# Kernel tuning notes

Hardware: AMD Instinct MI355X
Metric: run time of the kernel (lower is better)

The kernel has to match this reference:

```python
import jax, jax.numpy as jnp
import numpy as np

B, S, D = 4, 2048, 512
H, DK, DV = 8, 64, 64
LN_EPS = 1e-5


def setup_inputs() -> dict:
    key = jax.random.key(0)
    ks = jax.random.split(key, 9)
    inp = {
        "input_Q": jax.random.normal(ks[0], (B, S, D), jnp.float32),
        "input_K": jax.random.normal(ks[1], (B, S, D), jnp.float32),
        "input_V": jax.random.normal(ks[2], (B, S, D), jnp.float32),
        "attn_mask": jax.random.bernoulli(ks[3], 0.1, (B, S, S)),
        # weights stored [in, out] (math-equivalent to torch Linear's x @ W.T)
        "W_Q": jax.random.normal(ks[4], (D, H * DK), jnp.float32) * (1.0 / np.sqrt(D)),
        "W_K": jax.random.normal(ks[5], (D, H * DK), jnp.float32) * (1.0 / np.sqrt(D)),
        "W_V": jax.random.normal(ks[6], (D, H * DV), jnp.float32) * (1.0 / np.sqrt(D)),
        "W_fc": jax.random.normal(ks[7], (H * DV, D), jnp.float32) * (1.0 / np.sqrt(H * DV)),
        "ln_gamma": jnp.ones((D,), jnp.float32),
        "ln_beta": jnp.zeros((D,), jnp.float32),
    }
    return inp


def _mha(input_Q, input_K, input_V, attn_mask, W_Q, W_K, W_V, W_fc, ln_gamma, ln_beta):
    # project and split heads -> [B, H, S, d]
    Q = (input_Q @ W_Q).reshape(B, S, H, DK).transpose(0, 2, 1, 3)
    K = (input_K @ W_K).reshape(B, S, H, DK).transpose(0, 2, 1, 3)
    V = (input_V @ W_V).reshape(B, S, H, DV).transpose(0, 2, 1, 3)
    # scaled dot-product attention with masking (mask broadcast over heads)
    scores = jnp.einsum('bhqd,bhkd->bhqk', Q, K) / np.sqrt(DK)
    scores = jnp.where(attn_mask[:, None, :, :], -1e9, scores)
    attn = jax.nn.softmax(scores, axis=-1)
    context = jnp.einsum('bhqk,bhkd->bhqd', attn, V)
    context = context.transpose(0, 2, 1, 3).reshape(B, S, H * DV)
    out = context @ W_fc + input_Q  # fc + residual
    # LayerNorm over last dim
    mu = jnp.mean(out, axis=-1, keepdims=True)
    var = jnp.var(out, axis=-1, keepdims=True)
    normed = (out - mu) * jax.lax.rsqrt(var + LN_EPS) * ln_gamma + ln_beta
    return normed, attn


def reference(input_Q, input_K, input_V, attn_mask, W_Q, W_K, W_V, W_fc, ln_gamma, ln_beta):
    return _mha(input_Q, input_K, input_V, attn_mask, W_Q, W_K, W_V, W_fc, ln_gamma, ln_beta)
```

## Files before the change

kernel.cpp:

```cpp
#include <hip/hip_runtime.h>
#include <stdint.h>

typedef __attribute__((ext_vector_type(8))) short short8;
typedef __attribute__((ext_vector_type(4))) float f32x4;
typedef __attribute__((ext_vector_type(16))) float f32x16;
typedef __attribute__((ext_vector_type(4))) unsigned short ushort4v;
typedef __attribute__((ext_vector_type(4))) int int4v;

__device__ __forceinline__ unsigned short f2bf(float f) {
    union { float f; uint32_t u; } v; v.f = f;
    return (unsigned short)((v.u + 0x7FFFu + ((v.u >> 16) & 1u)) >> 16);
}
__device__ __forceinline__ float bf2f(unsigned short h) {
    union { uint32_t u; float f; } v; v.u = ((uint32_t)h) << 16;
    return v.f;
}

__global__ __launch_bounds__(256) void prep_wt_kernel(
    const float* __restrict__ W0, const float* __restrict__ W1,
    const float* __restrict__ W2, const float* __restrict__ W3,
    unsigned short* __restrict__ Wt)
{
    __shared__ unsigned short tile[64][66];
    const float* W = blockIdx.y == 0 ? W0 : blockIdx.y == 1 ? W1 : blockIdx.y == 2 ? W2 : W3;
    unsigned short* dst = Wt + (size_t)blockIdx.y * (512 * 512);
    const int k0 = (blockIdx.x >> 3) * 64;
    const int n0 = (blockIdx.x & 7) * 64;
    const int nx = threadIdx.x & 63;
    const int ty = threadIdx.x >> 6;
#pragma unroll
    for (int i = 0; i < 16; ++i) {
        const int kl = i * 4 + ty;
        tile[nx][kl] = f2bf(W[(size_t)(k0 + kl) * 512 + n0 + nx]);
    }
    __syncthreads();
#pragma unroll
    for (int i = 0; i < 16; ++i) {
        const int nl = i * 4 + ty;
        dst[(size_t)(n0 + nl) * 512 + k0 + nx] = tile[nl][nx];
    }
}

__global__ __launch_bounds__(256) void proj_kernel(
    const float* __restrict__ inQ, const float* __restrict__ inK, const float* __restrict__ inV,
    const unsigned short* __restrict__ Wt,
    unsigned short* __restrict__ outQ, unsigned short* __restrict__ outK,
    unsigned short* __restrict__ outVT)
{
    const int which = blockIdx.y;
    const float* inp = which == 0 ? inQ : which == 1 ? inK : inV;
    const unsigned short* Wtb = Wt + (size_t)which * (512 * 512);
    const int tid = threadIdx.x;
    const int wid = tid >> 6, l = tid & 63;
    const int rt = wid >> 1, ch = wid & 1;
    const int lrow = l & 15, g = l >> 4;
    const int rowbase = blockIdx.x * 32;
    const int arow = rowbase + rt * 16 + lrow;

    f32x4 acc[16];
#pragma unroll
    for (int t = 0; t < 16; ++t) acc[t] = (f32x4){0.f, 0.f, 0.f, 0.f};

    for (int k0 = 0; k0 < 512; k0 += 32) {
        const float* ap = inp + (size_t)arow * 512 + k0 + g * 8;
        float4 a0 = *(const float4*)ap;
        float4 a1 = *(const float4*)(ap + 4);
        short8 af;
        af[0] = (short)f2bf(a0.x); af[1] = (short)f2bf(a0.y);
        af[2] = (short)f2bf(a0.z); af[3] = (short)f2bf(a0.w);
        af[4] = (short)f2bf(a1.x); af[5] = (short)f2bf(a1.y);
        af[6] = (short)f2bf(a1.z); af[7] = (short)f2bf(a1.w);
#pragma unroll
        for (int t = 0; t < 16; ++t) {
            const int n = ch * 256 + t * 16 + lrow;
            short8 bf = *(const short8*)(Wtb + (size_t)n * 512 + k0 + g * 8);
            acc[t] = __builtin_amdgcn_mfma_f32_16x16x32_bf16(af, bf, acc[t], 0, 0, 0);
        }
    }

    if (which == 2) {
#pragma unroll
        for (int t = 0; t < 16; ++t) {
            const int n = ch * 256 + t * 16 + lrow;
            const int hh = n >> 6, dd = n & 63;
            const int row0 = rowbase + rt * 16 + g * 4;
            const int bb = row0 >> 11, s0 = row0 & 2047;
            ushort4v pk;
            pk[0] = f2bf(acc[t][0]); pk[1] = f2bf(acc[t][1]);
            pk[2] = f2bf(acc[t][2]); pk[3] = f2bf(acc[t][3]);
            *(ushort4v*)(outVT + ((size_t)(bb * 8 + hh) * 64 + dd) * 2048 + s0) = pk;
        }
    } else {
        unsigned short* dst = which == 0 ? outQ : outK;
#pragma unroll
        for (int t = 0; t < 16; ++t) {
            const int n = ch * 256 + t * 16 + lrow;
            const int hh = n >> 6, dd = n & 63;
#pragma unroll
            for (int r = 0; r < 4; ++r) {
                const int row = rowbase + rt * 16 + g * 4 + r;
                const int bb = row >> 11, s0 = row & 2047;
                dst[((size_t)(bb * 8 + hh) * 2048 + s0) * 64 + dd] = f2bf(acc[t][r]);
            }
        }
    }
}

__global__ __launch_bounds__(256, 4) void attn_kernel(
    const unsigned short* __restrict__ Qw, const unsigned short* __restrict__ Kw,
    const unsigned short* __restrict__ VT, const unsigned char* __restrict__ mask,
    float* __restrict__ attn_out, float* __restrict__ ctx)
{
    __shared__ float psum_lds[4][32];
    __shared__ float ctx_lds[4][32][67];

    const int L = blockIdx.x;
    const int xcd = L & 7, j = L >> 3;
    const int bh = xcd * 4 + (j >> 6);
    const int qb = j & 63;
    const int b = bh >> 3, h = bh & 7;
    const int qg0 = qb * 32;
    const int tid = threadIdx.x, wid = tid >> 6, l = tid & 63;
    const int lq = l & 31, hi = l >> 5;
    const float EXPC = 0.18033688011112042f;

    const unsigned short* qbase = Qw + ((size_t)bh * 2048 + qg0 + lq) * 64 + 8 * hi;
    short8 qf[4];
#pragma unroll
    for (int d4 = 0; d4 < 4; ++d4) qf[d4] = *(const short8*)(qbase + d4 * 16);

    const int k0w = wid * 512;
    const unsigned char* mbase = mask + ((size_t)b * 2048 + qg0 + lq) * 2048 + 4 * hi;
    const unsigned short* kwb = Kw + ((size_t)bh * 2048 + lq) * 64 + 8 * hi;

    float psum = 0.f;
    for (int t = 0; t < 16; ++t) {
        const int kb = k0w + t * 32;
        const unsigned short* kp = kwb + (size_t)kb * 64;
        short8 kf0 = *(const short8*)(kp);
        short8 kf1 = *(const short8*)(kp + 16);
        short8 kf2 = *(const short8*)(kp + 32);
        short8 kf3 = *(const short8*)(kp + 48);
        f32x16 sc = (f32x16)(0.f);
        sc = __builtin_amdgcn_mfma_f32_32x32x16_bf16(kf0, qf[0], sc, 0, 0, 0);
        sc = __builtin_amdgcn_mfma_f32_32x32x16_bf16(kf1, qf[1], sc, 0, 0, 0);
        sc = __builtin_amdgcn_mfma_f32_32x32x16_bf16(kf2, qf[2], sc, 0, 0, 0);
        sc = __builtin_amdgcn_mfma_f32_32x32x16_bf16(kf3, qf[3], sc, 0, 0, 0);
#pragma unroll
        for (int c2 = 0; c2 < 4; ++c2) {
            const uint32_t m4 = *(const uint32_t*)(mbase + kb + 8 * c2);
#pragma unroll
            for (int rr = 0; rr < 4; ++rr) {
                const float e = ((m4 >> (8 * rr)) & 255u) ? 0.f
                                : exp2f(sc[c2 * 4 + rr] * EXPC);
                psum += e;
            }
        }
    }
    psum += __shfl_xor(psum, 32);
    if (l < 32) psum_lds[wid][l] = psum;
    __syncthreads();
    const float rinv = 1.0f / (psum_lds[0][lq] + psum_lds[1][lq] +
                               psum_lds[2][lq] + psum_lds[3][lq]);

    f32x16 acc0 = (f32x16)(0.f), acc1 = (f32x16)(0.f);
    float* abase = attn_out + ((size_t)bh * 2048 + qg0 + lq) * 2048 + 4 * hi;
    const unsigned short* vb0 = VT + ((size_t)bh * 64 + lq) * 2048 + 8 * hi;
    const unsigned short* vb1 = vb0 + (size_t)32 * 2048;

    for (int t = 0; t < 16; ++t) {
        const int kb = k0w + t * 32;
        const unsigned short* kp = kwb + (size_t)kb * 64;
        short8 kf0 = *(const short8*)(kp);
        short8 kf1 = *(const short8*)(kp + 16);
        short8 kf2 = *(const short8*)(kp + 32);
        short8 kf3 = *(const short8*)(kp + 48);
        f32x16 sc = (f32x16)(0.f);
        sc = __builtin_amdgcn_mfma_f32_32x32x16_bf16(kf0, qf[0], sc, 0, 0, 0);
        sc = __builtin_amdgcn_mfma_f32_32x32x16_bf16(kf1, qf[1], sc, 0, 0, 0);
        sc = __builtin_amdgcn_mfma_f32_32x32x16_bf16(kf2, qf[2], sc, 0, 0, 0);
        sc = __builtin_amdgcn_mfma_f32_32x32x16_bf16(kf3, qf[3], sc, 0, 0, 0);

        float e[16];
#pragma unroll
        for (int c2 = 0; c2 < 4; ++c2) {
            const uint32_t m4 = *(const uint32_t*)(mbase + kb + 8 * c2);
#pragma unroll
            for (int rr = 0; rr < 4; ++rr) {
                e[c2 * 4 + rr] = ((m4 >> (8 * rr)) & 255u) ? 0.f
                                 : exp2f(sc[c2 * 4 + rr] * EXPC) * rinv;
            }
        }
#pragma unroll
        for (int c2 = 0; c2 < 4; ++c2) {
            float4 st = {e[c2 * 4 + 0], e[c2 * 4 + 1], e[c2 * 4 + 2], e[c2 * 4 + 3]};
            *(float4*)(abase + kb + 8 * c2) = st;
        }
#pragma unroll
        for (int kh = 0; kh < 2; ++kh) {
            const int cA = 2 * kh, cB = 2 * kh + 1;
            uint32_t w0 = (uint32_t)f2bf(e[4 * cA + 0]) | ((uint32_t)f2bf(e[4 * cA + 1]) << 16);
            uint32_t w1 = (uint32_t)f2bf(e[4 * cB + 0]) | ((uint32_t)f2bf(e[4 * cB + 1]) << 16);
            uint32_t w2 = (uint32_t)f2bf(e[4 * cA + 2]) | ((uint32_t)f2bf(e[4 * cA + 3]) << 16);
            uint32_t w3 = (uint32_t)f2bf(e[4 * cB + 2]) | ((uint32_t)f2bf(e[4 * cB + 3]) << 16);
            asm("v_permlane32_swap_b32 %0, %1" : "+v"(w0), "+v"(w1));
            asm("v_permlane32_swap_b32 %0, %1" : "+v"(w2), "+v"(w3));
            int4v pw = {(int)w0, (int)w2, (int)w1, (int)w3};
            short8 pb = *(short8*)&pw;
            const size_t voff = (size_t)(kb + 16 * kh);
            short8 v0 = *(const short8*)(vb0 + voff);
            short8 v1 = *(const short8*)(vb1 + voff);
            acc0 = __builtin_amdgcn_mfma_f32_32x32x16_bf16(v0, pb, acc0, 0, 0, 0);
            acc1 = __builtin_amdgcn_mfma_f32_32x32x16_bf16(v1, pb, acc1, 0, 0, 0);
        }
    }

#pragma unroll
    for (int r = 0; r < 16; ++r) {
        const int d = (r & 3) + 8 * (r >> 2) + 4 * hi;
        ctx_lds[wid][lq][d] = acc0[r];
        ctx_lds[wid][lq][d + 32] = acc1[r];
    }
    __syncthreads();
#pragma unroll
    for (int i = 0; i < 8; ++i) {
        const int idx = i * 256 + tid;
        const int q = idx >> 6, d = idx & 63;
        const float s = ctx_lds[0][q][d] + ctx_lds[1][q][d] +
                        ctx_lds[2][q][d] + ctx_lds[3][q][d];
        ctx[((size_t)b * 2048 + qg0 + q) * 512 + h * 64 + d] = s;
    }
}

__global__ __launch_bounds__(256) void fc_ln_kernel(
    const float* __restrict__ ctx, const unsigned short* __restrict__ Wtfc,
    const float* __restrict__ resid, const float* __restrict__ gamma,
    const float* __restrict__ beta, float* __restrict__ out)
{
    __shared__ float red[32][2][2];
    const int tid = threadIdx.x;
    const int wid = tid >> 6, l = tid & 63;
    const int rt = wid >> 1, ch = wid & 1;
    const int lrow = l & 15, g = l >> 4;
    const int rowbase = blockIdx.x * 32;
    const int arow = rowbase + rt * 16 + lrow;

    f32x4 acc[16];
#pragma unroll
    for (int t = 0; t < 16; ++t) acc[t] = (f32x4){0.f, 0.f, 0.f, 0.f};

    for (int k0 = 0; k0 < 512; k0 += 32) {
        const float* ap = ctx + (size_t)arow * 512 + k0 + g * 8;
        float4 a0 = *(const float4*)ap;
        float4 a1 = *(const float4*)(ap + 4);
        short8 af;
        af[0] = (short)f2bf(a0.x); af[1] = (short)f2bf(a0.y);
        af[2] = (short)f2bf(a0.z); af[3] = (short)f2bf(a0.w);
        af[4] = (short)f2bf(a1.x); af[5] = (short)f2bf(a1.y);
        af[6] = (short)f2bf(a1.z); af[7] = (short)f2bf(a1.w);
#pragma unroll
        for (int t = 0; t < 16; ++t) {
            const int n = ch * 256 + t * 16 + lrow;
            short8 bf = *(const short8*)(Wtfc + (size_t)n * 512 + k0 + g * 8);
            acc[t] = __builtin_amdgcn_mfma_f32_16x16x32_bf16(af, bf, acc[t], 0, 0, 0);
        }
    }

    float s1[4] = {0,0,0,0}, s2[4] = {0,0,0,0};
#pragma unroll
    for (int t = 0; t < 16; ++t) {
        const int n = ch * 256 + t * 16 + lrow;
#pragma unroll
        for (int r = 0; r < 4; ++r) {
            const int row = rowbase + rt * 16 + g * 4 + r;
            float v = acc[t][r] + resid[(size_t)row * 512 + n];
            acc[t][r] = v;
            s1[r] += v;
            s2[r] += v * v;
        }
    }
#pragma unroll
    for (int r = 0; r < 4; ++r) {
        s1[r] += __shfl_xor(s1[r], 1); s2[r] += __shfl_xor(s2[r], 1);
        s1[r] += __shfl_xor(s1[r], 2); s2[r] += __shfl_xor(s2[r], 2);
        s1[r] += __shfl_xor(s1[r], 4); s2[r] += __shfl_xor(s2[r], 4);
        s1[r] += __shfl_xor(s1[r], 8); s2[r] += __shfl_xor(s2[r], 8);
    }
    if (lrow == 0) {
#pragma unroll
        for (int r = 0; r < 4; ++r) {
            red[rt * 16 + g * 4 + r][ch][0] = s1[r];
            red[rt * 16 + g * 4 + r][ch][1] = s2[r];
        }
    }
    __syncthreads();
    float mean[4], rstd[4];
#pragma unroll
    for (int r = 0; r < 4; ++r) {
        const int rl = rt * 16 + g * 4 + r;
        const float S1 = red[rl][0][0] + red[rl][1][0];
        const float S2 = red[rl][0][1] + red[rl][1][1];
        mean[r] = S1 * (1.0f / 512.0f);
        const float var = S2 * (1.0f / 512.0f) - mean[r] * mean[r];
        rstd[r] = rsqrtf(var + 1e-5f);
    }
#pragma unroll
    for (int t = 0; t < 16; ++t) {
        const int n = ch * 256 + t * 16 + lrow;
        const float gm = gamma[n], bt = beta[n];
#pragma unroll
        for (int r = 0; r < 4; ++r) {
            const int row = rowbase + rt * 16 + g * 4 + r;
            out[(size_t)row * 512 + n] = (acc[t][r] - mean[r]) * rstd[r] * gm + bt;
        }
    }
}

extern "C" void kernel_launch(void* const* d_in, const int* in_sizes, int n_in,
                              void* d_out, int out_size, void* d_ws, size_t ws_size,
                              hipStream_t stream)
{
    (void)in_sizes; (void)n_in; (void)out_size; (void)ws_size;
    const float* inQ = (const float*)d_in[0];
    const float* inK = (const float*)d_in[1];
    const float* inV = (const float*)d_in[2];
    const unsigned char* mask = (const unsigned char*)d_in[3];
    const float* WQ  = (const float*)d_in[4];
    const float* WK  = (const float*)d_in[5];
    const float* WV  = (const float*)d_in[6];
    const float* Wfc = (const float*)d_in[7];
    const float* gamma = (const float*)d_in[8];
    const float* beta  = (const float*)d_in[9];

    char* ws = (char*)d_ws;
    unsigned short* wsQ   = (unsigned short*)(ws);
    unsigned short* wsK   = (unsigned short*)(ws + ((size_t)8  << 20));
    unsigned short* wsVT  = (unsigned short*)(ws + ((size_t)16 << 20));
    float*          wsCtx = (float*)         (ws + ((size_t)24 << 20));
    unsigned short* wsWt  = (unsigned short*)(ws + ((size_t)40 << 20));

    float* out_ln   = (float*)d_out;
    float* out_attn = out_ln + (size_t)4 * 2048 * 512;

    prep_wt_kernel<<<dim3(64, 4), dim3(256), 0, stream>>>(WQ, WK, WV, Wfc, wsWt);
    proj_kernel<<<dim3(256, 3), dim3(256), 0, stream>>>(inQ, inK, inV, wsWt, wsQ, wsK, wsVT);
    attn_kernel<<<dim3(2048), dim3(256), 0, stream>>>(wsQ, wsK, wsVT, mask,
                                                      out_attn, wsCtx);
    fc_ln_kernel<<<dim3(256), dim3(256), 0, stream>>>(wsCtx, wsWt + (size_t)3 * 512 * 512,
                                                      inQ, gamma, beta, out_ln);
}
```

Before: 1.002 ms.

## Split projection and fc grids, use raw exp/cvt asm, tree-reduce attention context

The projection kernel gains a second grid dimension that splits the output columns in half, and the fc+LayerNorm kernel processes 16 rows per block across four waves, doubling the block count of both GEMMs for better CU occupancy. In the attention kernel, exp2f is replaced by raw v_exp_f32 and bf16 packing by v_cvt_pk_bf16_f32, V fragments are loaded earlier in the loop, and the cross-wave context reduction becomes a two-step tree using smaller LDS with vectorized float4 stores. These changes aim to cut ALU work and LDS footprint. The cost is more redundant A-operand loads in the GEMMs and reliance on the unguarded hardware exp, which is less accurate.

```diff
diff --git a/kernel.cpp b/kernel.cpp
--- a/kernel.cpp
+++ b/kernel.cpp
@@ -14,6 +14,16 @@
 __device__ __forceinline__ float bf2f(unsigned short h) {
     union { uint32_t u; float f; } v; v.u = ((uint32_t)h) << 16;
     return v.f;
+}
+__device__ __forceinline__ float fexp2(float x) {
+    float r;
+    asm("v_exp_f32 %0, %1" : "=v"(r) : "v"(x));
+    return r;
+}
+__device__ __forceinline__ uint32_t cvtpk(float lo, float hi) {
+    uint32_t r;
+    asm("v_cvt_pk_bf16_f32 %0, %1, %2" : "=v"(r) : "v"(lo), "v"(hi));
+    return r;
 }
 
 __global__ __launch_bounds__(256) void prep_wt_kernel(
@@ -47,7 +57,7 @@
     unsigned short* __restrict__ outQ, unsigned short* __restrict__ outK,
     unsigned short* __restrict__ outVT)
 {
-    const int which = blockIdx.y;
+    const int which = blockIdx.z;
     const float* inp = which == 0 ? inQ : which == 1 ? inK : inV;
     const unsigned short* Wtb = Wt + (size_t)which * (512 * 512);
     const int tid = threadIdx.x;
@@ -55,11 +65,12 @@
     const int rt = wid >> 1, ch = wid & 1;
     const int lrow = l & 15, g = l >> 4;
     const int rowbase = blockIdx.x * 32;
+    const int nbase = blockIdx.y * 256 + ch * 128;
     const int arow = rowbase + rt * 16 + lrow;
 
-    f32x4 acc[16];
-#pragma unroll
-    for (int t = 0; t < 16; ++t) acc[t] = (f32x4){0.f, 0.f, 0.f, 0.f};
+    f32x4 acc[8];
+#pragma unroll
+    for (int t = 0; t < 8; ++t) acc[t] = (f32x4){0.f, 0.f, 0.f, 0.f};
 
     for (int k0 = 0; k0 < 512; k0 += 32) {
         const float* ap = inp + (size_t)arow * 512 + k0 + g * 8;
@@ -71,8 +82,8 @@
         af[4] = (short)f2bf(a1.x); af[5] = (short)f2bf(a1.y);
         af[6] = (short)f2bf(a1.z); af[7] = (short)f2bf(a1.w);
 #pragma unroll
-        for (int t = 0; t < 16; ++t) {
-            const int n = ch * 256 + t * 16 + lrow;
+        for (int t = 0; t < 8; ++t) {
+            const int n = nbase + t * 16 + lrow;
             short8 bf = *(const short8*)(Wtb + (size_t)n * 512 + k0 + g * 8);
             acc[t] = __builtin_amdgcn_mfma_f32_16x16x32_bf16(af, bf, acc[t], 0, 0, 0);
         }
@@ -80,8 +91,8 @@
 
     if (which == 2) {
 #pragma unroll
-        for (int t = 0; t < 16; ++t) {
-            const int n = ch * 256 + t * 16 + lrow;
+        for (int t = 0; t < 8; ++t) {
+            const int n = nbase + t * 16 + lrow;
             const int hh = n >> 6, dd = n & 63;
             const int row0 = rowbase + rt * 16 + g * 4;
             const int bb = row0 >> 11, s0 = row0 & 2047;
@@ -93,8 +104,8 @@
     } else {
         unsigned short* dst = which == 0 ? outQ : outK;
 #pragma unroll
-        for (int t = 0; t < 16; ++t) {
-            const int n = ch * 256 + t * 16 + lrow;
+        for (int t = 0; t < 8; ++t) {
+            const int n = nbase + t * 16 + lrow;
             const int hh = n >> 6, dd = n & 63;
 #pragma unroll
             for (int r = 0; r < 4; ++r) {
@@ -112,7 +123,8 @@
     float* __restrict__ attn_out, float* __restrict__ ctx)
 {
     __shared__ float psum_lds[4][32];
-    __shared__ float ctx_lds[4][32][67];
+    __shared__ float red0[32][68];
+    __shared__ float red1[32][68];
 
     const int L = blockIdx.x;
     const int xcd = L & 7, j = L >> 3;
@@ -151,9 +163,8 @@
             const uint32_t m4 = *(const uint32_t*)(mbase + kb + 8 * c2);
 #pragma unroll
             for (int rr = 0; rr < 4; ++rr) {
-                const float e = ((m4 >> (8 * rr)) & 255u) ? 0.f
-                                : exp2f(sc[c2 * 4 + rr] * EXPC);
-                psum += e;
+                const float ev = fexp2(sc[c2 * 4 + rr] * EXPC);
+                psum += ((m4 >> (8 * rr)) & 255u) ? 0.f : ev;
             }
         }
     }
@@ -175,6 +186,10 @@
         short8 kf1 = *(const short8*)(kp + 16);
         short8 kf2 = *(const short8*)(kp + 32);
         short8 kf3 = *(const short8*)(kp + 48);
+        short8 v00 = *(const short8*)(vb0 + kb);
+        short8 v01 = *(const short8*)(vb0 + kb + 16);
+        short8 v10 = *(const short8*)(vb1 + kb);
+        short8 v11 = *(const short8*)(vb1 + kb + 16);
         f32x16 sc = (f32x16)(0.f);
         sc = __builtin_amdgcn_mfma_f32_32x32x16_bf16(kf0, qf[0], sc, 0, 0, 0);
         sc = __builtin_amdgcn_mfma_f32_32x32x16_bf16(kf1, qf[1], sc, 0, 0, 0);
@@ -187,8 +202,8 @@
             const uint32_t m4 = *(const uint32_t*)(mbase + kb + 8 * c2);
 #pragma unroll
             for (int rr = 0; rr < 4; ++rr) {
-                e[c2 * 4 + rr] = ((m4 >> (8 * rr)) & 255u) ? 0.f
-                                 : exp2f(sc[c2 * 4 + rr] * EXPC) * rinv;
+                const float ev = fexp2(sc[c2 * 4 + rr] * EXPC) * rinv;
+                e[c2 * 4 + rr] = ((m4 >> (8 * rr)) & 255u) ? 0.f : ev;
             }
         }
 #pragma unroll
@@ -199,36 +214,66 @@
 #pragma unroll
         for (int kh = 0; kh < 2; ++kh) {
             const int cA = 2 * kh, cB = 2 * kh + 1;
-            uint32_t w0 = (uint32_t)f2bf(e[4 * cA + 0]) | ((uint32_t)f2bf(e[4 * cA + 1]) << 16);
-            uint32_t w1 = (uint32_t)f2bf(e[4 * cB + 0]) | ((uint32_t)f2bf(e[4 * cB + 1]) << 16);
-            uint32_t w2 = (uint32_t)f2bf(e[4 * cA + 2]) | ((uint32_t)f2bf(e[4 * cA + 3]) << 16);
-            uint32_t w3 = (uint32_t)f2bf(e[4 * cB + 2]) | ((uint32_t)f2bf(e[4 * cB + 3]) << 16);
+            uint32_t w0 = cvtpk(e[4 * cA + 0], e[4 * cA + 1]);
+            uint32_t w1 = cvtpk(e[4 * cB + 0], e[4 * cB + 1]);
+            uint32_t w2 = cvtpk(e[4 * cA + 2], e[4 * cA + 3]);
+            uint32_t w3 = cvtpk(e[4 * cB + 2], e[4 * cB + 3]);
             asm("v_permlane32_swap_b32 %0, %1" : "+v"(w0), "+v"(w1));
             asm("v_permlane32_swap_b32 %0, %1" : "+v"(w2), "+v"(w3));
             int4v pw = {(int)w0, (int)w2, (int)w1, (int)w3};
             short8 pb = *(short8*)&pw;
-            const size_t voff = (size_t)(kb + 16 * kh);
-            short8 v0 = *(const short8*)(vb0 + voff);
-            short8 v1 = *(const short8*)(vb1 + voff);
-            acc0 = __builtin_amdgcn_mfma_f32_32x32x16_bf16(v0, pb, acc0, 0, 0, 0);
-            acc1 = __builtin_amdgcn_mfma_f32_32x32x16_bf16(v1, pb, acc1, 0, 0, 0);
-        }
-    }
-
-#pragma unroll
-    for (int r = 0; r < 16; ++r) {
-        const int d = (r & 3) + 8 * (r >> 2) + 4 * hi;
-        ctx_lds[wid][lq][d] = acc0[r];
-        ctx_lds[wid][lq][d + 32] = acc1[r];
-    }
-    __syncthreads();
-#pragma unroll
-    for (int i = 0; i < 8; ++i) {
-        const int idx = i * 256 + tid;
-        const int q = idx >> 6, d = idx & 63;
-        const float s = ctx_lds[0][q][d] + ctx_lds[1][q][d] +
-                        ctx_lds[2][q][d] + ctx_lds[3][q][d];
-        ctx[((size_t)b * 2048 + qg0 + q) * 512 + h * 64 + d] = s;
+            short8 va = kh ? v01 : v00;
+            short8 vbt = kh ? v11 : v10;
+            acc0 = __builtin_amdgcn_mfma_f32_32x32x16_bf16(va, pb, acc0, 0, 0, 0);
+            acc1 = __builtin_amdgcn_mfma_f32_32x32x16_bf16(vbt, pb, acc1, 0, 0, 0);
+        }
+    }
+
+    if (wid >= 2) {
+        float (*rd)[68] = (wid == 2) ? red0 : red1;
+#pragma unroll
+        for (int c = 0; c < 4; ++c) {
+            const int d = 8 * c + 4 * hi;
+            *(float4*)&rd[lq][d]      = (float4){acc0[4*c+0], acc0[4*c+1], acc0[4*c+2], acc0[4*c+3]};
+            *(float4*)&rd[lq][d + 32] = (float4){acc1[4*c+0], acc1[4*c+1], acc1[4*c+2], acc1[4*c+3]};
+        }
+    }
+    __syncthreads();
+    if (wid < 2) {
+        float (*rd)[68] = (wid == 0) ? red0 : red1;
+#pragma unroll
+        for (int c = 0; c < 4; ++c) {
+            const int d = 8 * c + 4 * hi;
+            float4 p0 = *(const float4*)&rd[lq][d];
+            float4 p1 = *(const float4*)&rd[lq][d + 32];
+            acc0[4*c+0] += p0.x; acc0[4*c+1] += p0.y; acc0[4*c+2] += p0.z; acc0[4*c+3] += p0.w;
+            acc1[4*c+0] += p1.x; acc1[4*c+1] += p1.y; acc1[4*c+2] += p1.z; acc1[4*c+3] += p1.w;
+        }
+    }
+    __syncthreads();
+    if (wid == 1) {
+#pragma unroll
+        for (int c = 0; c < 4; ++c) {
+            const int d = 8 * c + 4 * hi;
+            *(float4*)&red1[lq][d]      = (float4){acc0[4*c+0], acc0[4*c+1], acc0[4*c+2], acc0[4*c+3]};
+            *(float4*)&red1[lq][d + 32] = (float4){acc1[4*c+0], acc1[4*c+1], acc1[4*c+2], acc1[4*c+3]};
+        }
+    }
+    __syncthreads();
+    if (wid == 0) {
+        float* cbase = ctx + ((size_t)b * 2048 + qg0 + lq) * 512 + h * 64;
+#pragma unroll
+        for (int c = 0; c < 4; ++c) {
+            const int d = 8 * c + 4 * hi;
+            float4 p0 = *(const float4*)&red1[lq][d];
+            float4 p1 = *(const float4*)&red1[lq][d + 32];
+            float4 s0 = {acc0[4*c+0] + p0.x, acc0[4*c+1] + p0.y,
+                         acc0[4*c+2] + p0.z, acc0[4*c+3] + p0.w};
+            float4 s1 = {acc1[4*c+0] + p1.x, acc1[4*c+1] + p1.y,
+                         acc1[4*c+2] + p1.z, acc1[4*c+3] + p1.w};
+            *(float4*)(cbase + d)      = s0;
+            *(float4*)(cbase + d + 32) = s1;
+        }
     }
 }
 
@@ -237,17 +282,16 @@
     const float* __restrict__ resid, const float* __restrict__ gamma,
     const float* __restrict__ beta, float* __restrict__ out)
 {
-    __shared__ float red[32][2][2];
+    __shared__ float red[16][4][2];
     const int tid = threadIdx.x;
-    const int wid = tid >> 6, l = tid & 63;
-    const int rt = wid >> 1, ch = wid & 1;
+    const int ch = tid >> 6, l = tid & 63;
     const int lrow = l & 15, g = l >> 4;
-    const int rowbase = blockIdx.x * 32;
-    const int arow = rowbase + rt * 16 + lrow;
-
-    f32x4 acc[16];
-#pragma unroll
-    for (int t = 0; t < 16; ++t) acc[t] = (f32x4){0.f, 0.f, 0.f, 0.f};
+    const int rowbase = blockIdx.x * 16;
+    const int arow = rowbase + lrow;
+
+    f32x4 acc[8];
+#pragma unroll
+    for (int t = 0; t < 8; ++t) acc[t] = (f32x4){0.f, 0.f, 0.f, 0.f};
 
     for (int k0 = 0; k0 < 512; k0 += 32) {
         const float* ap = ctx + (size_t)arow * 512 + k0 + g * 8;
@@ -259,8 +303,8 @@
         af[4] = (short)f2bf(a1.x); af[5] = (short)f2bf(a1.y);
         af[6] = (short)f2bf(a1.z); af[7] = (short)f2bf(a1.w);
 #pragma unroll
-        for (int t = 0; t < 16; ++t) {
-            const int n = ch * 256 + t * 16 + lrow;
+        for (int t = 0; t < 8; ++t) {
+            const int n = ch * 128 + t * 16 + lrow;
             short8 bf = *(const short8*)(Wtfc + (size_t)n * 512 + k0 + g * 8);
             acc[t] = __builtin_amdgcn_mfma_f32_16x16x32_bf16(af, bf, acc[t], 0, 0, 0);
         }
@@ -268,11 +312,11 @@
 
     float s1[4] = {0,0,0,0}, s2[4] = {0,0,0,0};
 #pragma unroll
-    for (int t = 0; t < 16; ++t) {
-        const int n = ch * 256 + t * 16 + lrow;
+    for (int t = 0; t < 8; ++t) {
+        const int n = ch * 128 + t * 16 + lrow;
 #pragma unroll
         for (int r = 0; r < 4; ++r) {
-            const int row = rowbase + rt * 16 + g * 4 + r;
+            const int row = rowbase + g * 4 + r;
             float v = acc[t][r] + resid[(size_t)row * 512 + n];
             acc[t][r] = v;
             s1[r] += v;
@@ -289,28 +333,28 @@
     if (lrow == 0) {
 #pragma unroll
         for (int r = 0; r < 4; ++r) {
-            red[rt * 16 + g * 4 + r][ch][0] = s1[r];
-            red[rt * 16 + g * 4 + r][ch][1] = s2[r];
+            red[g * 4 + r][ch][0] = s1[r];
+            red[g * 4 + r][ch][1] = s2[r];
         }
     }
     __syncthreads();
     float mean[4], rstd[4];
 #pragma unroll
     for (int r = 0; r < 4; ++r) {
-        const int rl = rt * 16 + g * 4 + r;
-        const float S1 = red[rl][0][0] + red[rl][1][0];
-        const float S2 = red[rl][0][1] + red[rl][1][1];
+        const int rl = g * 4 + r;
+        const float S1 = red[rl][0][0] + red[rl][1][0] + red[rl][2][0] + red[rl][3][0];
+        const float S2 = red[rl][0][1] + red[rl][1][1] + red[rl][2][1] + red[rl][3][1];
         mean[r] = S1 * (1.0f / 512.0f);
         const float var = S2 * (1.0f / 512.0f) - mean[r] * mean[r];
         rstd[r] = rsqrtf(var + 1e-5f);
     }
 #pragma unroll
-    for (int t = 0; t < 16; ++t) {
-        const int n = ch * 256 + t * 16 + lrow;
+    for (int t = 0; t < 8; ++t) {
+        const int n = ch * 128 + t * 16 + lrow;
         const float gm = gamma[n], bt = beta[n];
 #pragma unroll
         for (int r = 0; r < 4; ++r) {
-            const int row = rowbase + rt * 16 + g * 4 + r;
+            const int row = rowbase + g * 4 + r;
             out[(size_t)row * 512 + n] = (acc[t][r] - mean[r]) * rstd[r] * gm + bt;
         }
     }
@@ -343,9 +387,10 @@
     float* out_attn = out_ln + (size_t)4 * 2048 * 512;
 
     prep_wt_kernel<<<dim3(64, 4), dim3(256), 0, stream>>>(WQ, WK, WV, Wfc, wsWt);
-    proj_kernel<<<dim3(256, 3), dim3(256), 0, stream>>>(inQ, inK, inV, wsWt, wsQ, wsK, wsVT);
+    proj_kernel<<<dim3(256, 2, 3), dim3(256), 0, stream>>>(inQ, inK, inV, wsWt,
+                                                           wsQ, wsK, wsVT);
     attn_kernel<<<dim3(2048), dim3(256), 0, stream>>>(wsQ, wsK, wsVT, mask,
                                                       out_attn, wsCtx);
-    fc_ln_kernel<<<dim3(256), dim3(256), 0, stream>>>(wsCtx, wsWt + (size_t)3 * 512 * 512,
+    fc_ln_kernel<<<dim3(512), dim3(256), 0, stream>>>(wsCtx, wsWt + (size_t)3 * 512 * 512,
                                                       inQ, gamma, beta, out_ln);
 }
```

Result: slower. 1.059 ms (+5.7%).
